# Performance work log

Measured on AMD Instinct MI355X. Metric: run time of the kernel, lower is better.

Reference implementation:

```python
import jax, jax.numpy as jnp
import numpy as np

NUM_HEADS = 12


def _build_mask(N, unseen_size, dtype):
    # Columns for the last `unseen_size` tokens are masked (-inf) for every
    # query row EXCEPT the diagonal entries in that block (each unseen token
    # may attend to itself). Matches the original Python-loop construction.
    idx = jnp.arange(N)
    col_unseen = idx[None, :] >= (N - unseen_size)
    off_diag = idx[:, None] != idx[None, :]
    return jnp.where(col_unseen & off_diag, -jnp.inf, jnp.asarray(0.0, dtype))


def reference(x, w_qkv, w_proj, b_proj, unseen_size):
    B, N, C = x.shape
    H = NUM_HEADS
    d = C // H
    scale = d ** -0.5
    # qkv: (B,N,3C) -> (3,B,H,N,d)
    qkv = (x @ w_qkv.T).reshape(B, N, 3, H, d).transpose(2, 0, 3, 1, 4)
    q, k, v = qkv[0], qkv[1], qkv[2]
    attn = jnp.einsum('bhqd,bhkd->bhqk', q, k) * scale
    attn = attn + _build_mask(N, unseen_size, attn.dtype)  # broadcast (N,N)
    attn = jax.nn.softmax(attn, axis=-1)
    out = jnp.einsum('bhqk,bhkd->bhqd', attn, v)
    out = out.transpose(0, 2, 1, 3).reshape(B, N, C)
    return out @ w_proj.T + b_proj


def setup_inputs() -> dict:
    key = jax.random.key(0)
    k1, k2, k3 = jax.random.split(key, 3)
    B, N, C = 2, 2048, 768
    x = jax.random.normal(k1, (B, N, C), dtype=jnp.float32)
    w_qkv = jax.random.normal(k2, (3 * C, C), dtype=jnp.float32) * (C ** -0.5)
    w_proj = jax.random.normal(k3, (C, C), dtype=jnp.float32) * (C ** -0.5)
    b_proj = jnp.zeros((C,), dtype=jnp.float32)
    return {"x": x, "w_qkv": w_qkv, "w_proj": w_proj, "b_proj": b_proj,
            "unseen_size": 512}
```

## Files before the change

### kernel.cpp

```cpp
#include <hip/hip_runtime.h>
#include <math.h>

#define NH 12
#define DH 64
#define NSEQ 2048
#define NB 2
#define CDIM 768
#define NVIS 1536

typedef _Float16 half8 __attribute__((ext_vector_type(8)));
typedef _Float16 half4 __attribute__((ext_vector_type(4)));
typedef float floatx4 __attribute__((ext_vector_type(4)));

static constexpr size_t SZ_X    = (size_t)NB*NSEQ*CDIM;
static constexpr size_t SZ_WQKV = (size_t)3*CDIM*CDIM;
static constexpr size_t SZ_WP   = (size_t)CDIM*CDIM;
static constexpr size_t SZ_HEAD = (size_t)NB*NH*NSEQ*DH;

#define GLOAD_LDS16(gp, lp) \
  __builtin_amdgcn_global_load_lds((const __attribute__((address_space(1))) void*)(gp), \
                                   (__attribute__((address_space(3))) void*)(lp), 16, 0, 0)

__global__ __launch_bounds__(256) void convert_kernel(
    const float* __restrict__ x, const float* __restrict__ wqkv, const float* __restrict__ wp,
    _Float16* __restrict__ xb, _Float16* __restrict__ wqkvb, _Float16* __restrict__ wpb)
{
  size_t idx = ((size_t)blockIdx.x*256 + threadIdx.x)*4;
  const float* src; _Float16* dst; size_t off;
  if (idx < SZ_X)                        { src = x;    dst = xb;    off = idx; }
  else if (idx < SZ_X+SZ_WQKV)           { src = wqkv; dst = wqkvb; off = idx - SZ_X; }
  else if (idx < SZ_X+SZ_WQKV+SZ_WP)     { src = wp;   dst = wpb;   off = idx - SZ_X - SZ_WQKV; }
  else return;
  float4 v = *reinterpret_cast<const float4*>(src + off);
  _Float16 o[4] = {(_Float16)v.x,(_Float16)v.y,(_Float16)v.z,(_Float16)v.w};
  *reinterpret_cast<uint2*>(dst + off) = *reinterpret_cast<uint2*>(o);
}

template<int MODE, int BN>
__global__ __launch_bounds__(256) void gemm_bt(
    const _Float16* __restrict__ A, const _Float16* __restrict__ Bt,
    const float* __restrict__ bias,
    _Float16* __restrict__ qb, _Float16* __restrict__ kb, _Float16* __restrict__ vb,
    float* __restrict__ outp)
{
  constexpr int K = CDIM;
  constexpr int BM = 128, BK = 32;
  constexpr int MI = (BN == 128) ? 4 : 2;
  constexpr int NI = 4;
  __shared__ _Float16 As[BM*BK];
  __shared__ _Float16 Bs[BN*BK];
  const int tid = threadIdx.x;
  const int lane = tid & 63, wid = tid >> 6;
  const int l15 = lane & 15, quad = lane >> 4;
  const int wm = (BN == 128) ? (wid >> 1)*64 : wid*32;
  const int wn = (BN == 128) ? (wid & 1)*64 : 0;
  const int tileN = blockIdx.x*BN, tileM = blockIdx.y*BM;
  const int lrow = lane >> 2, lchunk = lane & 3;
  const int gcol = ((lchunk ^ (lrow >> 1)) & 3)*8;
  const _Float16* gA0 = A  + (size_t)(tileM + wid*32      + lrow)*K + gcol;
  const _Float16* gA1 = A  + (size_t)(tileM + wid*32 + 16 + lrow)*K + gcol;
  const _Float16* gB0 = Bt + (size_t)(tileN + ((BN==128) ? wid*32 : wid*16) + lrow)*K + gcol;
  const _Float16* gB1 = Bt + (size_t)(tileN + wid*32 + 16 + lrow)*K + gcol;
  _Float16* lA0 = As + (wid*32)*BK;
  _Float16* lA1 = As + (wid*32 + 16)*BK;
  _Float16* lB0 = Bs + ((BN==128) ? wid*32 : wid*16)*BK;
  _Float16* lB1 = Bs + (wid*32 + 16)*BK;
  const int cp = ((quad ^ (l15 >> 1)) & 3)*8;
  floatx4 acc[MI][NI] = {};
  for (int k0 = 0; k0 < K; k0 += BK) {
    __syncthreads();
    GLOAD_LDS16(gA0 + k0, lA0);
    GLOAD_LDS16(gA1 + k0, lA1);
    GLOAD_LDS16(gB0 + k0, lB0);
    if (BN == 128) GLOAD_LDS16(gB1 + k0, lB1);
    __syncthreads();
    half8 af[MI], bfr[NI];
    #pragma unroll
    for (int mi = 0; mi < MI; mi++)
      af[mi] = *reinterpret_cast<const half8*>(&As[(wm + mi*16 + l15)*BK + cp]);
    #pragma unroll
    for (int ni = 0; ni < NI; ni++)
      bfr[ni] = *reinterpret_cast<const half8*>(&Bs[(wn + ni*16 + l15)*BK + cp]);
    #pragma unroll
    for (int mi = 0; mi < MI; mi++)
      #pragma unroll
      for (int ni = 0; ni < NI; ni++)
        acc[mi][ni] = __builtin_amdgcn_mfma_f32_16x16x32_f16(af[mi], bfr[ni], acc[mi][ni], 0,0,0);
  }
  #pragma unroll
  for (int mi = 0; mi < MI; mi++)
    #pragma unroll
    for (int ni = 0; ni < NI; ni++) {
      int n = tileN + wn + ni*16 + l15;
      int m0 = tileM + wm + mi*16 + quad*4;
      if (MODE == 0) {
        int part = n / CDIM, rem = n - part*CDIM;
        int h = rem >> 6, dd = rem & 63;
        int b = m0 >> 11, i0 = m0 & 2047;
        if (part == 2) {
          half4 pk = {(_Float16)acc[mi][ni][0], (_Float16)acc[mi][ni][1],
                      (_Float16)acc[mi][ni][2], (_Float16)acc[mi][ni][3]};
          *reinterpret_cast<half4*>(&vb[(((size_t)b*NH + h)*DH + dd)*NSEQ + i0]) = pk;
        } else {
          _Float16* dst = part ? kb : qb;
          float sc = part ? 1.0f : 0.125f*1.44269504f;
          #pragma unroll
          for (int r = 0; r < 4; r++)
            dst[(((size_t)b*NH + h)*NSEQ + i0 + r)*DH + dd] = (_Float16)(acc[mi][ni][r]*sc);
        }
      } else {
        #pragma unroll
        for (int r = 0; r < 4; r++)
          outp[(size_t)(m0 + r)*CDIM + n] = acc[mi][ni][r] + bias[n];
      }
    }
}

__global__ __launch_bounds__(256, 3) void fa_kernel(
    const _Float16* __restrict__ qg, const _Float16* __restrict__ kg,
    const _Float16* __restrict__ vtg, _Float16* __restrict__ og)
{
  constexpr int LDP = 72;
  __shared__ _Float16 Ps[2][64*LDP];
  __shared__ float Ls[4*64];
  const int blk = blockIdx.x;
  const int idx = blk >> 3;
  const int bh = (blk & 7)*3 + (idx % 3);
  const int qbase = (idx / 3) * 64;
  const int tid = threadIdx.x;
  const int lane = tid & 63, w = tid >> 6;
  const int l15 = lane & 15, quad = lane >> 4;
  const _Float16* qp  = qg  + (size_t)bh*NSEQ*DH;
  const _Float16* kbp = kg  + (size_t)bh*NSEQ*DH;
  const _Float16* vbp = vtg + (size_t)bh*DH*NSEQ;
  half8 qf[4][2];
  #pragma unroll
  for (int g = 0; g < 4; g++)
    #pragma unroll
    for (int c = 0; c < 2; c++)
      qf[g][c] = *reinterpret_cast<const half8*>(qp + (size_t)(qbase + g*16 + l15)*DH + c*32 + quad*8);
  const _Float16* kRow = kbp + (size_t)(w*16 + l15)*DH + quad*8;
  const _Float16* vRow = vbp + (size_t)(w*16 + l15)*NSEQ + quad*8;
  floatx4 o[4] = {};
  float lsum[4] = {0.f, 0.f, 0.f, 0.f};

  half8 kcur0 = *reinterpret_cast<const half8*>(kRow);
  half8 kcur1 = *reinterpret_cast<const half8*>(kRow + 32);
  {
    floatx4 st[4] = {};
    #pragma unroll
    for (int g = 0; g < 4; g++) {
      st[g] = __builtin_amdgcn_mfma_f32_16x16x32_f16(kcur0, qf[g][0], st[g], 0,0,0);
      st[g] = __builtin_amdgcn_mfma_f32_16x16x32_f16(kcur1, qf[g][1], st[g], 0,0,0);
    }
    #pragma unroll
    for (int g = 0; g < 4; g++) {
      float e0 = __builtin_exp2f(st[g][0]), e1 = __builtin_exp2f(st[g][1]);
      float e2 = __builtin_exp2f(st[g][2]), e3 = __builtin_exp2f(st[g][3]);
      lsum[g] += (e0+e1)+(e2+e3);
      half4 pk = {(_Float16)e0,(_Float16)e1,(_Float16)e2,(_Float16)e3};
      *reinterpret_cast<half4*>(&Ps[0][(g*16+l15)*LDP + w*16 + quad*4]) = pk;
    }
  }
  half8 vcur0 = *reinterpret_cast<const half8*>(vRow);
  half8 vcur1 = *reinterpret_cast<const half8*>(vRow + 32);
  kcur0 = *reinterpret_cast<const half8*>(kRow + (size_t)64*DH);
  kcur1 = *reinterpret_cast<const half8*>(kRow + (size_t)64*DH + 32);

  for (int t = 0; t < 23; t++) {
    const int tk = (t + 2 < 24) ? t + 2 : 0;
    half8 kn0 = *reinterpret_cast<const half8*>(kRow + (size_t)tk*64*DH);
    half8 kn1 = *reinterpret_cast<const half8*>(kRow + (size_t)tk*64*DH + 32);
    half8 vn0 = *reinterpret_cast<const half8*>(vRow + (t+1)*64);
    half8 vn1 = *reinterpret_cast<const half8*>(vRow + (t+1)*64 + 32);
    floatx4 st[4] = {};
    #pragma unroll
    for (int g = 0; g < 4; g++) {
      st[g] = __builtin_amdgcn_mfma_f32_16x16x32_f16(kcur0, qf[g][0], st[g], 0,0,0);
      st[g] = __builtin_amdgcn_mfma_f32_16x16x32_f16(kcur1, qf[g][1], st[g], 0,0,0);
    }
    half4 pk[4];
    #pragma unroll
    for (int g = 0; g < 4; g++) {
      float e0 = __builtin_exp2f(st[g][0]), e1 = __builtin_exp2f(st[g][1]);
      float e2 = __builtin_exp2f(st[g][2]), e3 = __builtin_exp2f(st[g][3]);
      lsum[g] += (e0+e1)+(e2+e3);
      pk[g] = half4{(_Float16)e0,(_Float16)e1,(_Float16)e2,(_Float16)e3};
    }
    __syncthreads();
    #pragma unroll
    for (int g = 0; g < 4; g++)
      *reinterpret_cast<half4*>(&Ps[(t+1)&1][(g*16+l15)*LDP + w*16 + quad*4]) = pk[g];
    #pragma unroll
    for (int g = 0; g < 4; g++) {
      half8 pb0 = *reinterpret_cast<const half8*>(&Ps[t&1][(g*16+l15)*LDP + quad*8]);
      half8 pb1 = *reinterpret_cast<const half8*>(&Ps[t&1][(g*16+l15)*LDP + 32 + quad*8]);
      o[g] = __builtin_amdgcn_mfma_f32_16x16x32_f16(vcur0, pb0, o[g], 0,0,0);
      o[g] = __builtin_amdgcn_mfma_f32_16x16x32_f16(vcur1, pb1, o[g], 0,0,0);
    }
    kcur0 = kn0; kcur1 = kn1; vcur0 = vn0; vcur1 = vn1;
  }
  __syncthreads();
  #pragma unroll
  for (int g = 0; g < 4; g++) {
    half8 pb0 = *reinterpret_cast<const half8*>(&Ps[1][(g*16+l15)*LDP + quad*8]);
    half8 pb1 = *reinterpret_cast<const half8*>(&Ps[1][(g*16+l15)*LDP + 32 + quad*8]);
    o[g] = __builtin_amdgcn_mfma_f32_16x16x32_f16(vcur0, pb0, o[g], 0,0,0);
    o[g] = __builtin_amdgcn_mfma_f32_16x16x32_f16(vcur1, pb1, o[g], 0,0,0);
  }
  #pragma unroll
  for (int g = 0; g < 4; g++) {
    lsum[g] += __shfl_xor(lsum[g], 16);
    lsum[g] += __shfl_xor(lsum[g], 32);
  }
  if (lane < 16) {
    #pragma unroll
    for (int g = 0; g < 4; g++) Ls[w*64 + g*16 + lane] = lsum[g];
  }
  __syncthreads();
  float den[4];
  #pragma unroll
  for (int g = 0; g < 4; g++)
    den[g] = Ls[g*16+l15] + Ls[64+g*16+l15] + Ls[128+g*16+l15] + Ls[192+g*16+l15];
  if (qbase >= NVIS) {
    #pragma unroll
    for (int g = 0; g < 4; g++) {
      half8 kd0 = *reinterpret_cast<const half8*>(kbp + (size_t)(qbase + g*16 + l15)*DH + quad*8);
      half8 kd1 = *reinterpret_cast<const half8*>(kbp + (size_t)(qbase + g*16 + l15)*DH + 32 + quad*8);
      float pd = 0.f;
      #pragma unroll
      for (int j = 0; j < 8; j++)
        pd += (float)qf[g][0][j]*(float)kd0[j] + (float)qf[g][1][j]*(float)kd1[j];
      pd += __shfl_xor(pd, 16);
      pd += __shfl_xor(pd, 32);
      float e = __builtin_exp2f(pd);
      den[g] += e;
      #pragma unroll
      for (int r = 0; r < 4; r++)
        o[g][r] += e * (float)vbp[(size_t)(w*16+quad*4+r)*NSEQ + qbase + g*16 + l15];
    }
  }
  const int b = bh / NH, h = bh - b*NH;
  #pragma unroll
  for (int g = 0; g < 4; g++) {
    float inv = 1.0f / den[g];
    half4 pk = {(_Float16)(o[g][0]*inv), (_Float16)(o[g][1]*inv),
                (_Float16)(o[g][2]*inv), (_Float16)(o[g][3]*inv)};
    size_t oaddr = ((size_t)b*NSEQ + qbase + g*16 + l15)*CDIM + h*DH + w*16 + quad*4;
    *reinterpret_cast<half4*>(&og[oaddr]) = pk;
  }
}

extern "C" void kernel_launch(void* const* d_in, const int* in_sizes, int n_in,
                              void* d_out, int out_size, void* d_ws, size_t ws_size,
                              hipStream_t stream) {
  (void)in_sizes; (void)n_in; (void)out_size; (void)ws_size;
  const float* x     = (const float*)d_in[0];
  const float* wqkv  = (const float*)d_in[1];
  const float* wproj = (const float*)d_in[2];
  const float* bproj = (const float*)d_in[3];

  _Float16* xb    = (_Float16*)d_ws;
  _Float16* wqkvb = xb + SZ_X;
  _Float16* wpb   = wqkvb + SZ_WQKV;
  _Float16* qb    = wpb + SZ_WP;
  _Float16* kb    = qb + SZ_HEAD;
  _Float16* vb    = kb + SZ_HEAD;
  _Float16* ob    = vb + SZ_HEAD;
  float* outp = (float*)d_out;

  size_t total = SZ_X + SZ_WQKV + SZ_WP;
  int cblocks = (int)((total/4 + 255)/256);
  convert_kernel<<<cblocks, 256, 0, stream>>>(x, wqkv, wproj, xb, wqkvb, wpb);
  gemm_bt<0,128><<<dim3(3*CDIM/128, NB*NSEQ/128), 256, 0, stream>>>(xb, wqkvb, nullptr, qb, kb, vb, nullptr);
  fa_kernel<<<NB*NH*(NSEQ/64), 256, 0, stream>>>(qb, kb, vb, ob);
  gemm_bt<1,64><<<dim3(CDIM/64, NB*NSEQ/128), 256, 0, stream>>>(ob, wpb, bproj, nullptr, nullptr, nullptr, outp);
}
```

Measured before the change: 160.9 us.

## Retile PV stage as 2x2 warp grid with XOR-swizzled P buffer

The P·V stage is repartitioned so each warp computes a 32-query by 32-dim output tile instead of 64 queries by 16 dims. This halves the shared-memory reads of P per warp, since each P fragment now feeds two MFMAs, at the cost of loading twice as many V rows per warp from global memory. The padded P buffer is replaced by an unpadded 64x64 layout with an XOR swizzle to avoid bank conflicts, which also reduces LDS usage. The diagonal correction and output-store code are remapped to the new tile ownership.

```diff
diff --git a/kernel.cpp b/kernel.cpp
--- a/kernel.cpp
+++ b/kernel.cpp
@@ -120,8 +120,7 @@
     const _Float16* __restrict__ qg, const _Float16* __restrict__ kg,
     const _Float16* __restrict__ vtg, _Float16* __restrict__ og)
 {
-  constexpr int LDP = 72;
-  __shared__ _Float16 Ps[2][64*LDP];
+  __shared__ _Float16 Ps[2][64*64];
   __shared__ float Ls[4*64];
   const int blk = blockIdx.x;
   const int idx = blk >> 3;
@@ -130,6 +129,8 @@
   const int tid = threadIdx.x;
   const int lane = tid & 63, w = tid >> 6;
   const int l15 = lane & 15, quad = lane >> 4;
+  const int wq = w & 1, wd = w >> 1;
+  const int sw = (l15 & 7) << 3;
   const _Float16* qp  = qg  + (size_t)bh*NSEQ*DH;
   const _Float16* kbp = kg  + (size_t)bh*NSEQ*DH;
   const _Float16* vbp = vtg + (size_t)bh*DH*NSEQ;
@@ -139,10 +140,14 @@
     #pragma unroll
     for (int c = 0; c < 2; c++)
       qf[g][c] = *reinterpret_cast<const half8*>(qp + (size_t)(qbase + g*16 + l15)*DH + c*32 + quad*8);
-  const _Float16* kRow = kbp + (size_t)(w*16 + l15)*DH + quad*8;
-  const _Float16* vRow = vbp + (size_t)(w*16 + l15)*NSEQ + quad*8;
-  floatx4 o[4] = {};
+  const _Float16* kRow  = kbp + (size_t)(w*16 + l15)*DH + quad*8;
+  const _Float16* vRowA = vbp + (size_t)(wd*32 + l15)*NSEQ + quad*8;
+  const _Float16* vRowB = vRowA + (size_t)16*NSEQ;
+  floatx4 o[2][2] = {};
   float lsum[4] = {0.f, 0.f, 0.f, 0.f};
+  const int pws  = (w*16 + quad*4) ^ sw;
+  const int prd0 = (quad*8) ^ sw;
+  const int prd1 = (32 + quad*8) ^ sw;
 
   half8 kcur0 = *reinterpret_cast<const half8*>(kRow);
   half8 kcur1 = *reinterpret_cast<const half8*>(kRow + 32);
@@ -159,11 +164,13 @@
       float e2 = __builtin_exp2f(st[g][2]), e3 = __builtin_exp2f(st[g][3]);
       lsum[g] += (e0+e1)+(e2+e3);
       half4 pk = {(_Float16)e0,(_Float16)e1,(_Float16)e2,(_Float16)e3};
-      *reinterpret_cast<half4*>(&Ps[0][(g*16+l15)*LDP + w*16 + quad*4]) = pk;
-    }
-  }
-  half8 vcur0 = *reinterpret_cast<const half8*>(vRow);
-  half8 vcur1 = *reinterpret_cast<const half8*>(vRow + 32);
+      *reinterpret_cast<half4*>(&Ps[0][(g*16+l15)*64 + pws]) = pk;
+    }
+  }
+  half8 vcA0 = *reinterpret_cast<const half8*>(vRowA);
+  half8 vcA1 = *reinterpret_cast<const half8*>(vRowA + 32);
+  half8 vcB0 = *reinterpret_cast<const half8*>(vRowB);
+  half8 vcB1 = *reinterpret_cast<const half8*>(vRowB + 32);
   kcur0 = *reinterpret_cast<const half8*>(kRow + (size_t)64*DH);
   kcur1 = *reinterpret_cast<const half8*>(kRow + (size_t)64*DH + 32);
 
@@ -171,8 +178,10 @@
     const int tk = (t + 2 < 24) ? t + 2 : 0;
     half8 kn0 = *reinterpret_cast<const half8*>(kRow + (size_t)tk*64*DH);
     half8 kn1 = *reinterpret_cast<const half8*>(kRow + (size_t)tk*64*DH + 32);
-    half8 vn0 = *reinterpret_cast<const half8*>(vRow + (t+1)*64);
-    half8 vn1 = *reinterpret_cast<const half8*>(vRow + (t+1)*64 + 32);
+    half8 vnA0 = *reinterpret_cast<const half8*>(vRowA + (t+1)*64);
+    half8 vnA1 = *reinterpret_cast<const half8*>(vRowA + (t+1)*64 + 32);
+    half8 vnB0 = *reinterpret_cast<const half8*>(vRowB + (t+1)*64);
+    half8 vnB1 = *reinterpret_cast<const half8*>(vRowB + (t+1)*64 + 32);
     floatx4 st[4] = {};
     #pragma unroll
     for (int g = 0; g < 4; g++) {
@@ -190,23 +199,30 @@
     __syncthreads();
     #pragma unroll
     for (int g = 0; g < 4; g++)
-      *reinterpret_cast<half4*>(&Ps[(t+1)&1][(g*16+l15)*LDP + w*16 + quad*4]) = pk[g];
-    #pragma unroll
-    for (int g = 0; g < 4; g++) {
-      half8 pb0 = *reinterpret_cast<const half8*>(&Ps[t&1][(g*16+l15)*LDP + quad*8]);
-      half8 pb1 = *reinterpret_cast<const half8*>(&Ps[t&1][(g*16+l15)*LDP + 32 + quad*8]);
-      o[g] = __builtin_amdgcn_mfma_f32_16x16x32_f16(vcur0, pb0, o[g], 0,0,0);
-      o[g] = __builtin_amdgcn_mfma_f32_16x16x32_f16(vcur1, pb1, o[g], 0,0,0);
-    }
-    kcur0 = kn0; kcur1 = kn1; vcur0 = vn0; vcur1 = vn1;
+      *reinterpret_cast<half4*>(&Ps[(t+1)&1][(g*16+l15)*64 + pws]) = pk[g];
+    #pragma unroll
+    for (int qg = 0; qg < 2; qg++) {
+      const _Float16* pb = &Ps[t&1][(wq*32 + qg*16 + l15)*64];
+      half8 pb0 = *reinterpret_cast<const half8*>(pb + prd0);
+      half8 pb1 = *reinterpret_cast<const half8*>(pb + prd1);
+      o[0][qg] = __builtin_amdgcn_mfma_f32_16x16x32_f16(vcA0, pb0, o[0][qg], 0,0,0);
+      o[0][qg] = __builtin_amdgcn_mfma_f32_16x16x32_f16(vcA1, pb1, o[0][qg], 0,0,0);
+      o[1][qg] = __builtin_amdgcn_mfma_f32_16x16x32_f16(vcB0, pb0, o[1][qg], 0,0,0);
+      o[1][qg] = __builtin_amdgcn_mfma_f32_16x16x32_f16(vcB1, pb1, o[1][qg], 0,0,0);
+    }
+    kcur0 = kn0; kcur1 = kn1;
+    vcA0 = vnA0; vcA1 = vnA1; vcB0 = vnB0; vcB1 = vnB1;
   }
   __syncthreads();
   #pragma unroll
-  for (int g = 0; g < 4; g++) {
-    half8 pb0 = *reinterpret_cast<const half8*>(&Ps[1][(g*16+l15)*LDP + quad*8]);
-    half8 pb1 = *reinterpret_cast<const half8*>(&Ps[1][(g*16+l15)*LDP + 32 + quad*8]);
-    o[g] = __builtin_amdgcn_mfma_f32_16x16x32_f16(vcur0, pb0, o[g], 0,0,0);
-    o[g] = __builtin_amdgcn_mfma_f32_16x16x32_f16(vcur1, pb1, o[g], 0,0,0);
+  for (int qg = 0; qg < 2; qg++) {
+    const _Float16* pb = &Ps[1][(wq*32 + qg*16 + l15)*64];
+    half8 pb0 = *reinterpret_cast<const half8*>(pb + prd0);
+    half8 pb1 = *reinterpret_cast<const half8*>(pb + prd1);
+    o[0][qg] = __builtin_amdgcn_mfma_f32_16x16x32_f16(vcA0, pb0, o[0][qg], 0,0,0);
+    o[0][qg] = __builtin_amdgcn_mfma_f32_16x16x32_f16(vcA1, pb1, o[0][qg], 0,0,0);
+    o[1][qg] = __builtin_amdgcn_mfma_f32_16x16x32_f16(vcB0, pb0, o[1][qg], 0,0,0);
+    o[1][qg] = __builtin_amdgcn_mfma_f32_16x16x32_f16(vcB1, pb1, o[1][qg], 0,0,0);
   }
   #pragma unroll
   for (int g = 0; g < 4; g++) {
@@ -224,30 +240,37 @@
     den[g] = Ls[g*16+l15] + Ls[64+g*16+l15] + Ls[128+g*16+l15] + Ls[192+g*16+l15];
   if (qbase >= NVIS) {
     #pragma unroll
-    for (int g = 0; g < 4; g++) {
-      half8 kd0 = *reinterpret_cast<const half8*>(kbp + (size_t)(qbase + g*16 + l15)*DH + quad*8);
-      half8 kd1 = *reinterpret_cast<const half8*>(kbp + (size_t)(qbase + g*16 + l15)*DH + 32 + quad*8);
+    for (int qg = 0; qg < 2; qg++) {
+      const int gq = wq*2 + qg;
+      half8 kd0 = *reinterpret_cast<const half8*>(kbp + (size_t)(qbase + gq*16 + l15)*DH + quad*8);
+      half8 kd1 = *reinterpret_cast<const half8*>(kbp + (size_t)(qbase + gq*16 + l15)*DH + 32 + quad*8);
       float pd = 0.f;
       #pragma unroll
       for (int j = 0; j < 8; j++)
-        pd += (float)qf[g][0][j]*(float)kd0[j] + (float)qf[g][1][j]*(float)kd1[j];
+        pd += (float)qf[gq][0][j]*(float)kd0[j] + (float)qf[gq][1][j]*(float)kd1[j];
       pd += __shfl_xor(pd, 16);
       pd += __shfl_xor(pd, 32);
       float e = __builtin_exp2f(pd);
-      den[g] += e;
+      den[gq] += e;
       #pragma unroll
-      for (int r = 0; r < 4; r++)
-        o[g][r] += e * (float)vbp[(size_t)(w*16+quad*4+r)*NSEQ + qbase + g*16 + l15];
+      for (int dg = 0; dg < 2; dg++)
+        #pragma unroll
+        for (int r = 0; r < 4; r++)
+          o[dg][qg][r] += e * (float)vbp[(size_t)(wd*32 + dg*16 + quad*4 + r)*NSEQ + qbase + gq*16 + l15];
     }
   }
   const int b = bh / NH, h = bh - b*NH;
   #pragma unroll
-  for (int g = 0; g < 4; g++) {
-    float inv = 1.0f / den[g];
-    half4 pk = {(_Float16)(o[g][0]*inv), (_Float16)(o[g][1]*inv),
-                (_Float16)(o[g][2]*inv), (_Float16)(o[g][3]*inv)};
-    size_t oaddr = ((size_t)b*NSEQ + qbase + g*16 + l15)*CDIM + h*DH + w*16 + quad*4;
-    *reinterpret_cast<half4*>(&og[oaddr]) = pk;
+  for (int qg = 0; qg < 2; qg++) {
+    float inv = 1.0f / den[wq*2 + qg];
+    #pragma unroll
+    for (int dg = 0; dg < 2; dg++) {
+      half4 pk = {(_Float16)(o[dg][qg][0]*inv), (_Float16)(o[dg][qg][1]*inv),
+                  (_Float16)(o[dg][qg][2]*inv), (_Float16)(o[dg][qg][3]*inv)};
+      size_t oaddr = ((size_t)b*NSEQ + qbase + wq*32 + qg*16 + l15)*CDIM
+                   + h*DH + wd*32 + dg*16 + quad*4;
+      *reinterpret_cast<half4*>(&og[oaddr]) = pk;
+    }
   }
 }
 
```

After: 190.4 us. 1.18x slower.

## Give each wave its own query rows in attention, removing block-wide syncs

Applied to the files above, without the earlier changes.

The attention kernel is reorganized so each wave owns 16 query rows and walks all key tiles itself, rather than the four waves splitting each key tile and sharing P through LDS. This removes the per-iteration __syncthreads and the cross-wave row-sum reduction, and uses a private XOR-swizzled LDS tile per wave for the P transpose. K fragments are double-buffered in registers and s_setprio is raised around the MFMA bursts. In exchange every wave now loads the full K and V tiles itself, so global or L2 traffic per block is four times higher, and register pressure rises.

```diff
diff --git a/kernel.cpp b/kernel.cpp
--- a/kernel.cpp
+++ b/kernel.cpp
@@ -120,9 +120,7 @@
     const _Float16* __restrict__ qg, const _Float16* __restrict__ kg,
     const _Float16* __restrict__ vtg, _Float16* __restrict__ og)
 {
-  constexpr int LDP = 72;
-  __shared__ _Float16 Ps[2][64*LDP];
-  __shared__ float Ls[4*64];
+  __shared__ _Float16 Ps[4][16*64];
   const int blk = blockIdx.x;
   const int idx = blk >> 3;
   const int bh = (blk & 7)*3 + (idx % 3);
@@ -130,123 +128,114 @@
   const int tid = threadIdx.x;
   const int lane = tid & 63, w = tid >> 6;
   const int l15 = lane & 15, quad = lane >> 4;
+  const int sw = (l15 & 7) << 3;
+  const int qrow = qbase + w*16 + l15;
   const _Float16* qp  = qg  + (size_t)bh*NSEQ*DH;
   const _Float16* kbp = kg  + (size_t)bh*NSEQ*DH;
   const _Float16* vbp = vtg + (size_t)bh*DH*NSEQ;
-  half8 qf[4][2];
-  #pragma unroll
-  for (int g = 0; g < 4; g++)
+  _Float16* myP = Ps[w];
+  half8 qf[2];
+  #pragma unroll
+  for (int c = 0; c < 2; c++)
+    qf[c] = *reinterpret_cast<const half8*>(qp + (size_t)qrow*DH + c*32 + quad*8);
+  const _Float16* kT = kbp + (size_t)l15*DH + quad*8;
+  const _Float16* vT = vbp + (size_t)l15*NSEQ + quad*8;
+  const int prd0 = (quad*8) ^ sw;
+  const int prd1 = (32 + quad*8) ^ sw;
+
+  floatx4 o[4] = {};
+  float lsum = 0.f;
+
+  half8 ka[4][2], kb2[4][2];
+  #pragma unroll
+  for (int kg2 = 0; kg2 < 4; kg2++)
     #pragma unroll
     for (int c = 0; c < 2; c++)
-      qf[g][c] = *reinterpret_cast<const half8*>(qp + (size_t)(qbase + g*16 + l15)*DH + c*32 + quad*8);
-  const _Float16* kRow = kbp + (size_t)(w*16 + l15)*DH + quad*8;
-  const _Float16* vRow = vbp + (size_t)(w*16 + l15)*NSEQ + quad*8;
-  floatx4 o[4] = {};
-  float lsum[4] = {0.f, 0.f, 0.f, 0.f};
-
-  half8 kcur0 = *reinterpret_cast<const half8*>(kRow);
-  half8 kcur1 = *reinterpret_cast<const half8*>(kRow + 32);
-  {
-    floatx4 st[4] = {};
-    #pragma unroll
-    for (int g = 0; g < 4; g++) {
-      st[g] = __builtin_amdgcn_mfma_f32_16x16x32_f16(kcur0, qf[g][0], st[g], 0,0,0);
-      st[g] = __builtin_amdgcn_mfma_f32_16x16x32_f16(kcur1, qf[g][1], st[g], 0,0,0);
-    }
-    #pragma unroll
-    for (int g = 0; g < 4; g++) {
-      float e0 = __builtin_exp2f(st[g][0]), e1 = __builtin_exp2f(st[g][1]);
-      float e2 = __builtin_exp2f(st[g][2]), e3 = __builtin_exp2f(st[g][3]);
-      lsum[g] += (e0+e1)+(e2+e3);
-      half4 pk = {(_Float16)e0,(_Float16)e1,(_Float16)e2,(_Float16)e3};
-      *reinterpret_cast<half4*>(&Ps[0][(g*16+l15)*LDP + w*16 + quad*4]) = pk;
-    }
-  }
-  half8 vcur0 = *reinterpret_cast<const half8*>(vRow);
-  half8 vcur1 = *reinterpret_cast<const half8*>(vRow + 32);
-  kcur0 = *reinterpret_cast<const half8*>(kRow + (size_t)64*DH);
-  kcur1 = *reinterpret_cast<const half8*>(kRow + (size_t)64*DH + 32);
-
-  for (int t = 0; t < 23; t++) {
-    const int tk = (t + 2 < 24) ? t + 2 : 0;
-    half8 kn0 = *reinterpret_cast<const half8*>(kRow + (size_t)tk*64*DH);
-    half8 kn1 = *reinterpret_cast<const half8*>(kRow + (size_t)tk*64*DH + 32);
-    half8 vn0 = *reinterpret_cast<const half8*>(vRow + (t+1)*64);
-    half8 vn1 = *reinterpret_cast<const half8*>(vRow + (t+1)*64 + 32);
-    floatx4 st[4] = {};
-    #pragma unroll
-    for (int g = 0; g < 4; g++) {
-      st[g] = __builtin_amdgcn_mfma_f32_16x16x32_f16(kcur0, qf[g][0], st[g], 0,0,0);
-      st[g] = __builtin_amdgcn_mfma_f32_16x16x32_f16(kcur1, qf[g][1], st[g], 0,0,0);
-    }
-    half4 pk[4];
-    #pragma unroll
-    for (int g = 0; g < 4; g++) {
-      float e0 = __builtin_exp2f(st[g][0]), e1 = __builtin_exp2f(st[g][1]);
-      float e2 = __builtin_exp2f(st[g][2]), e3 = __builtin_exp2f(st[g][3]);
-      lsum[g] += (e0+e1)+(e2+e3);
-      pk[g] = half4{(_Float16)e0,(_Float16)e1,(_Float16)e2,(_Float16)e3};
-    }
-    __syncthreads();
-    #pragma unroll
-    for (int g = 0; g < 4; g++)
-      *reinterpret_cast<half4*>(&Ps[(t+1)&1][(g*16+l15)*LDP + w*16 + quad*4]) = pk[g];
-    #pragma unroll
-    for (int g = 0; g < 4; g++) {
-      half8 pb0 = *reinterpret_cast<const half8*>(&Ps[t&1][(g*16+l15)*LDP + quad*8]);
-      half8 pb1 = *reinterpret_cast<const half8*>(&Ps[t&1][(g*16+l15)*LDP + 32 + quad*8]);
-      o[g] = __builtin_amdgcn_mfma_f32_16x16x32_f16(vcur0, pb0, o[g], 0,0,0);
-      o[g] = __builtin_amdgcn_mfma_f32_16x16x32_f16(vcur1, pb1, o[g], 0,0,0);
-    }
-    kcur0 = kn0; kcur1 = kn1; vcur0 = vn0; vcur1 = vn1;
-  }
-  __syncthreads();
-  #pragma unroll
-  for (int g = 0; g < 4; g++) {
-    half8 pb0 = *reinterpret_cast<const half8*>(&Ps[1][(g*16+l15)*LDP + quad*8]);
-    half8 pb1 = *reinterpret_cast<const half8*>(&Ps[1][(g*16+l15)*LDP + 32 + quad*8]);
-    o[g] = __builtin_amdgcn_mfma_f32_16x16x32_f16(vcur0, pb0, o[g], 0,0,0);
-    o[g] = __builtin_amdgcn_mfma_f32_16x16x32_f16(vcur1, pb1, o[g], 0,0,0);
-  }
-  #pragma unroll
-  for (int g = 0; g < 4; g++) {
-    lsum[g] += __shfl_xor(lsum[g], 16);
-    lsum[g] += __shfl_xor(lsum[g], 32);
-  }
-  if (lane < 16) {
-    #pragma unroll
-    for (int g = 0; g < 4; g++) Ls[w*64 + g*16 + lane] = lsum[g];
-  }
-  __syncthreads();
-  float den[4];
-  #pragma unroll
-  for (int g = 0; g < 4; g++)
-    den[g] = Ls[g*16+l15] + Ls[64+g*16+l15] + Ls[128+g*16+l15] + Ls[192+g*16+l15];
+      ka[kg2][c] = *reinterpret_cast<const half8*>(kT + (size_t)kg2*16*DH + c*32);
+
+#define FA_ITER(T, CUR, NXT) {                                                    \
+    const _Float16* vt = vT + (size_t)(T)*64;                                     \
+    half8 vf0[2][2];                                                              \
+    _Pragma("unroll")                                                             \
+    for (int dg = 0; dg < 2; dg++)                                                \
+      _Pragma("unroll")                                                           \
+      for (int c = 0; c < 2; c++)                                                 \
+        vf0[dg][c] = *reinterpret_cast<const half8*>(vt + (size_t)dg*16*NSEQ + c*32); \
+    floatx4 st[4] = {};                                                           \
+    __builtin_amdgcn_s_setprio(1);                                                \
+    _Pragma("unroll")                                                             \
+    for (int kg2 = 0; kg2 < 4; kg2++) {                                           \
+      st[kg2] = __builtin_amdgcn_mfma_f32_16x16x32_f16(CUR[kg2][0], qf[0], st[kg2], 0,0,0); \
+      st[kg2] = __builtin_amdgcn_mfma_f32_16x16x32_f16(CUR[kg2][1], qf[1], st[kg2], 0,0,0); \
+    }                                                                             \
+    __builtin_amdgcn_s_setprio(0);                                                \
+    const _Float16* kt = kT + (size_t)((T)+1)*64*DH;                              \
+    _Pragma("unroll")                                                             \
+    for (int kg2 = 0; kg2 < 4; kg2++)                                             \
+      _Pragma("unroll")                                                           \
+      for (int c = 0; c < 2; c++)                                                 \
+        NXT[kg2][c] = *reinterpret_cast<const half8*>(kt + (size_t)kg2*16*DH + c*32); \
+    _Pragma("unroll")                                                             \
+    for (int kg2 = 0; kg2 < 4; kg2++) {                                           \
+      float e0 = __builtin_exp2f(st[kg2][0]), e1 = __builtin_exp2f(st[kg2][1]);   \
+      float e2 = __builtin_exp2f(st[kg2][2]), e3 = __builtin_exp2f(st[kg2][3]);   \
+      lsum += (e0+e1)+(e2+e3);                                                    \
+      half4 pk = {(_Float16)e0,(_Float16)e1,(_Float16)e2,(_Float16)e3};           \
+      *reinterpret_cast<half4*>(&myP[l15*64 + ((kg2*16 + quad*4) ^ sw)]) = pk;    \
+    }                                                                             \
+    half8 vf1[2][2];                                                              \
+    _Pragma("unroll")                                                             \
+    for (int dg = 0; dg < 2; dg++)                                                \
+      _Pragma("unroll")                                                           \
+      for (int c = 0; c < 2; c++)                                                 \
+        vf1[dg][c] = *reinterpret_cast<const half8*>(vt + (size_t)(dg+2)*16*NSEQ + c*32); \
+    half8 pb0 = *reinterpret_cast<const half8*>(&myP[l15*64 + prd0]);             \
+    half8 pb1 = *reinterpret_cast<const half8*>(&myP[l15*64 + prd1]);             \
+    __builtin_amdgcn_s_setprio(1);                                                \
+    o[0] = __builtin_amdgcn_mfma_f32_16x16x32_f16(vf0[0][0], pb0, o[0], 0,0,0);   \
+    o[0] = __builtin_amdgcn_mfma_f32_16x16x32_f16(vf0[0][1], pb1, o[0], 0,0,0);   \
+    o[1] = __builtin_amdgcn_mfma_f32_16x16x32_f16(vf0[1][0], pb0, o[1], 0,0,0);   \
+    o[1] = __builtin_amdgcn_mfma_f32_16x16x32_f16(vf0[1][1], pb1, o[1], 0,0,0);   \
+    o[2] = __builtin_amdgcn_mfma_f32_16x16x32_f16(vf1[0][0], pb0, o[2], 0,0,0);   \
+    o[2] = __builtin_amdgcn_mfma_f32_16x16x32_f16(vf1[0][1], pb1, o[2], 0,0,0);   \
+    o[3] = __builtin_amdgcn_mfma_f32_16x16x32_f16(vf1[1][0], pb0, o[3], 0,0,0);   \
+    o[3] = __builtin_amdgcn_mfma_f32_16x16x32_f16(vf1[1][1], pb1, o[3], 0,0,0);   \
+    __builtin_amdgcn_s_setprio(0);                                                \
+  }
+
+  for (int t = 0; t < 24; t += 2) {
+    FA_ITER(t,   ka,  kb2);
+    FA_ITER(t+1, kb2, ka);
+  }
+#undef FA_ITER
+
+  lsum += __shfl_xor(lsum, 16);
+  lsum += __shfl_xor(lsum, 32);
+  float den = lsum;
   if (qbase >= NVIS) {
-    #pragma unroll
-    for (int g = 0; g < 4; g++) {
-      half8 kd0 = *reinterpret_cast<const half8*>(kbp + (size_t)(qbase + g*16 + l15)*DH + quad*8);
-      half8 kd1 = *reinterpret_cast<const half8*>(kbp + (size_t)(qbase + g*16 + l15)*DH + 32 + quad*8);
-      float pd = 0.f;
-      #pragma unroll
-      for (int j = 0; j < 8; j++)
-        pd += (float)qf[g][0][j]*(float)kd0[j] + (float)qf[g][1][j]*(float)kd1[j];
-      pd += __shfl_xor(pd, 16);
-      pd += __shfl_xor(pd, 32);
-      float e = __builtin_exp2f(pd);
-      den[g] += e;
+    half8 kd0 = *reinterpret_cast<const half8*>(kbp + (size_t)qrow*DH + quad*8);
+    half8 kd1 = *reinterpret_cast<const half8*>(kbp + (size_t)qrow*DH + 32 + quad*8);
+    float pd = 0.f;
+    #pragma unroll
+    for (int j = 0; j < 8; j++)
+      pd += (float)qf[0][j]*(float)kd0[j] + (float)qf[1][j]*(float)kd1[j];
+    pd += __shfl_xor(pd, 16);
+    pd += __shfl_xor(pd, 32);
+    float e = __builtin_exp2f(pd);
+    den += e;
+    #pragma unroll
+    for (int dg = 0; dg < 4; dg++)
       #pragma unroll
       for (int r = 0; r < 4; r++)
-        o[g][r] += e * (float)vbp[(size_t)(w*16+quad*4+r)*NSEQ + qbase + g*16 + l15];
-    }
+        o[dg][r] += e * (float)vbp[(size_t)(dg*16 + quad*4 + r)*NSEQ + qrow];
   }
   const int b = bh / NH, h = bh - b*NH;
-  #pragma unroll
-  for (int g = 0; g < 4; g++) {
-    float inv = 1.0f / den[g];
-    half4 pk = {(_Float16)(o[g][0]*inv), (_Float16)(o[g][1]*inv),
-                (_Float16)(o[g][2]*inv), (_Float16)(o[g][3]*inv)};
-    size_t oaddr = ((size_t)b*NSEQ + qbase + g*16 + l15)*CDIM + h*DH + w*16 + quad*4;
+  float inv = 1.0f / den;
+  #pragma unroll
+  for (int dg = 0; dg < 4; dg++) {
+    half4 pk = {(_Float16)(o[dg][0]*inv), (_Float16)(o[dg][1]*inv),
+                (_Float16)(o[dg][2]*inv), (_Float16)(o[dg][3]*inv)};
+    size_t oaddr = ((size_t)b*NSEQ + qrow)*CDIM + h*DH + dg*16 + quad*4;
     *reinterpret_cast<half4*>(&og[oaddr]) = pk;
   }
 }
```

New measurement: 250.1 us. 55.5% more time.
